# Kernel tuning notes

Measured on AMD Instinct MI355X. Metric: run time of the kernel, lower is better.

Reference implementation:

```python
import jax, jax.numpy as jnp
import numpy as np

N_NODES = 100000
N_EDGES = 3200000
C, H, F = 512, 256, 64


def spmm(edge_row, edge_col, edge_val, Z):
    # (A @ Z)[i] = sum over edges e with row[e]==i of val[e] * Z[col[e]]
    msgs = edge_val[:, None] * Z[edge_col]  # [E, d]
    return jax.ops.segment_sum(msgs, edge_row, num_segments=N_NODES)


def setup_inputs() -> dict:
    key = jax.random.key(0)
    k1, k2, k3, k4, k5, k6, k7 = jax.random.split(key, 7)
    X = jax.random.normal(k1, (N_NODES, C), dtype=jnp.float32)
    edge_row = jax.random.randint(k2, (N_EDGES,), 0, N_NODES, dtype=jnp.int32)
    edge_col = jax.random.randint(k3, (N_EDGES,), 0, N_NODES, dtype=jnp.int32)
    edge_val = jax.random.uniform(k4, (N_EDGES,), dtype=jnp.float32)
    W0 = jax.random.normal(k5, (C, H), dtype=jnp.float32) * (C ** -0.5)
    Wh1 = jax.random.normal(k6, (H, H), dtype=jnp.float32) * (H ** -0.5)
    W1 = jax.random.normal(k7, (H, F), dtype=jnp.float32) * (H ** -0.5)
    return {"X": X, "edge_row": edge_row, "edge_col": edge_col,
            "edge_val": edge_val, "W0": W0, "Wh1": Wh1, "W1": W1}


def reference(X, edge_row, edge_col, edge_val, W0, Wh1, W1):
    # layer 0: relu(A @ (X W0))   (dropout=0 -> identity)
    Z = jax.nn.relu(spmm(edge_row, edge_col, edge_val, X @ W0))
    # hidden layers (num_layers - 2 = 1)
    Z = jax.nn.relu(spmm(edge_row, edge_col, edge_val, Z @ Wh1))
    # output layer: softmax(A @ (Z W1), axis=-1)
    Z = jax.nn.softmax(spmm(edge_row, edge_col, edge_val, Z @ W1), axis=-1)
    return Z
```

## Files before the change

### kernel.cpp

```cpp
#include <hip/hip_runtime.h>
#include <cstdint>
#include <cstddef>


#define SCAN_B 1024

typedef __attribute__((ext_vector_type(8))) short short8_t;
typedef __attribute__((ext_vector_type(4))) short short4_t;
typedef __attribute__((ext_vector_type(4))) float f32x4;

__device__ __forceinline__ short bf16_hi(float x) {
    union { float f; unsigned u; } c; c.f = x;
    return (short)(c.u >> 16);
}
__device__ __forceinline__ float bf16_f32(short h) {
    union { float f; unsigned u; } c; c.u = ((unsigned)(unsigned short)h) << 16;
    return c.f;
}

__device__ __forceinline__ void gload_lds16(const void* g, void* l) {
    __builtin_amdgcn_global_load_lds(
        (const __attribute__((address_space(1))) void*)g,
        (__attribute__((address_space(3))) void*)l, 16, 0, 0);
}

#define GBAR() asm volatile("s_barrier" ::: "memory")
#define LGKM0() asm volatile("s_waitcnt lgkmcnt(0)" ::: "memory")

__device__ __forceinline__ void wait_vm(int n) {
    switch (n) {
        case 0:  asm volatile("s_waitcnt vmcnt(0)"  ::: "memory"); break;
        case 6:  asm volatile("s_waitcnt vmcnt(6)"  ::: "memory"); break;
        case 8:  asm volatile("s_waitcnt vmcnt(8)"  ::: "memory"); break;
        default: asm volatile("s_waitcnt vmcnt(10)" ::: "memory"); break;
    }
}


__global__ __launch_bounds__(256) void count_xcd_k(const int* __restrict__ row,
                                                   int* __restrict__ deg,
                                                   int E, int gsz) {
    const int g = blockIdx.x & 7;
    const int lo = g * gsz, hi = lo + gsz;
    const int tidg = (blockIdx.x >> 3) * 256 + threadIdx.x;
    const int T = (gridDim.x >> 3) * 256;
    const int E4 = E >> 2;
    for (int c = tidg; c < E4; c += T) {
        int4 r = *(const int4*)&row[c * 4];
        if (r.x >= lo && r.x < hi) atomicAdd(&deg[r.x], 1);
        if (r.y >= lo && r.y < hi) atomicAdd(&deg[r.y], 1);
        if (r.z >= lo && r.z < hi) atomicAdd(&deg[r.z], 1);
        if (r.w >= lo && r.w < hi) atomicAdd(&deg[r.w], 1);
    }
    for (int e = E4 * 4 + tidg; e < E; e += T) {
        int r = row[e];
        if (r >= lo && r < hi) atomicAdd(&deg[r], 1);
    }
}

__global__ __launch_bounds__(SCAN_B) void scan1_k(const int* __restrict__ deg,
                                                  int* __restrict__ part,
                                                  int* __restrict__ bsum, int n) {
    __shared__ int buf[SCAN_B];
    int tid = threadIdx.x;
    int i = blockIdx.x * SCAN_B + tid;
    int v = (i < n) ? ((deg[i] + 3) & ~3) : 0;
    buf[tid] = v;
    __syncthreads();
    for (int off = 1; off < SCAN_B; off <<= 1) {
        int y = (tid >= off) ? buf[tid - off] : 0;
        __syncthreads();
        buf[tid] += y;
        __syncthreads();
    }
    if (i < n) part[i] = buf[tid] - v;
    if (tid == SCAN_B - 1) bsum[blockIdx.x] = buf[tid];
}

__global__ __launch_bounds__(128) void scan2_k(int* __restrict__ bsum, int nb) {
    __shared__ int buf[128];
    int tid = threadIdx.x;
    int v = (tid < nb) ? bsum[tid] : 0;
    buf[tid] = v;
    __syncthreads();
    for (int off = 1; off < 128; off <<= 1) {
        int y = (tid >= off) ? buf[tid - off] : 0;
        __syncthreads();
        buf[tid] += y;
        __syncthreads();
    }
    if (tid < nb) bsum[tid] = buf[tid] - v;
    if (tid == nb - 1) bsum[nb] = buf[tid];
}

__global__ __launch_bounds__(SCAN_B) void scan3_k(int* __restrict__ rowptr,
                                                  const int* __restrict__ bsum,
                                                  int* __restrict__ cursor, int n, int nb) {
    int i = blockIdx.x * SCAN_B + threadIdx.x;
    if (i < n) {
        int v = rowptr[i] + bsum[blockIdx.x];
        rowptr[i] = v;
        cursor[i] = v;
    }
    if (i == 0) rowptr[n] = bsum[nb];
}

__global__ __launch_bounds__(256) void scatter_xcd_k(const int* __restrict__ row,
                                                     const int* __restrict__ col,
                                                     const float* __restrict__ val,
                                                     int* __restrict__ cursor,
                                                     int2* __restrict__ ecv,
                                                     int E, int gsz) {
    const int g = blockIdx.x & 7;
    const int lo = g * gsz, hi = lo + gsz;
    const int tidg = (blockIdx.x >> 3) * 256 + threadIdx.x;
    const int T = (gridDim.x >> 3) * 256;
    const int E8 = E >> 3;
    for (int c = tidg; c < E8; c += T) {
        const int e = c * 8;
        int4   r0 = *(const int4*)&row[e];
        int4   r1 = *(const int4*)&row[e + 4];
        int4   c0 = *(const int4*)&col[e];
        int4   c1 = *(const int4*)&col[e + 4];
        float4 v0 = *(const float4*)&val[e];
        float4 v1 = *(const float4*)&val[e + 4];
        int   rr[8] = {r0.x, r0.y, r0.z, r0.w, r1.x, r1.y, r1.z, r1.w};
        int   cc[8] = {c0.x, c0.y, c0.z, c0.w, c1.x, c1.y, c1.z, c1.w};
        float vv[8] = {v0.x, v0.y, v0.z, v0.w, v1.x, v1.y, v1.z, v1.w};
        int p[8];
#pragma unroll
        for (int j = 0; j < 8; ++j)
            p[j] = (rr[j] >= lo && rr[j] < hi) ? atomicAdd(&cursor[rr[j]], 1) : -1;
#pragma unroll
        for (int j = 0; j < 8; ++j)
            if (p[j] >= 0) ecv[p[j]] = make_int2(cc[j], __float_as_int(vv[j]));
    }
    for (int e = E8 * 8 + tidg; e < E; e += T) {
        int r = row[e];
        if (r >= lo && r < hi) {
            int p = atomicAdd(&cursor[r], 1);
            ecv[p] = make_int2(col[e], __float_as_int(val[e]));
        }
    }
}

__global__ __launch_bounds__(256) void pad_fill_k(const int* __restrict__ cursor,
                                                  const int* __restrict__ rowptr,
                                                  int2* __restrict__ ecv, int N) {
    int r = blockIdx.x * 256 + threadIdx.x;
    if (r < N) {
        int q = cursor[r], e = rowptr[r + 1];
        for (; q < e; ++q) ecv[q] = make_int2(0, 0);
    }
}


__global__ void split_w_k(const float* __restrict__ W, short* __restrict__ Bhl,
                          int K, int M) {
    int i = blockIdx.x * 256 + threadIdx.x;
    if (i >= K * M) return;
    int k = i / M, m = i - k * M;
    float x = W[i];
    short hi = bf16_hi(x);
    float r = x - bf16_f32(hi);
    short lo = bf16_hi(r);
    int g = k >> 3, j = k & 7;
    Bhl[(size_t)m * (2 * K) + 16 * g + j] = hi;
    Bhl[(size_t)m * (2 * K) + 16 * g + 8 + j] = lo;
}


template <int K, int BN, int NWR, int NWC, bool AF32>
__global__ __launch_bounds__(256) void gemm_hl(const void* __restrict__ Av,
                                               const short* __restrict__ Bhl,
                                               short* __restrict__ ZQ,
                                               float* __restrict__ scl, int N) {
    constexpr int BM = 64 * NWR;
    constexpr int NF = BN / NWC / 16;
    constexpr int NT = K / 32;
    constexpr int LB = BN / 8 / 4;
    constexpr int LA = AF32 ? 0 : BM / 8 / 4;
    constexpr int L  = LA + LB;
    __shared__ short Ald[2][BM * 64];
    __shared__ short Bld[2][BN * 64];

    const int tid = threadIdx.x, lane = tid & 63, w = tid >> 6;
    const int wr = w / NWC, wc = w % NWC;
    const int row0 = blockIdx.x * BM;
    const int l8 = lane >> 3;
    const int sx = (lane & 7) ^ l8;

    const short* Ahl = (const short*)Av;
    const float* Af  = (const float*)Av;
    const int arow = tid >> 2, aq = tid & 3;
    const int akey = arow & 7;

    f32x4 acc[4][NF] = {};

    auto stageB = [&](int t, int b) {
#pragma unroll
        for (int ch = w; ch < BN / 8; ch += 4)
            gload_lds16(Bhl + (size_t)(ch * 8 + l8) * (2 * K) + (size_t)t * 64 + sx * 8,
                        &Bld[b][ch * 512]);
    };
    auto stageAg = [&](int t, int b) {
#pragma unroll
        for (int ch = w; ch < BM / 8; ch += 4)
            gload_lds16(Ahl + (size_t)(row0 + ch * 8 + l8) * (2 * K) + (size_t)t * 64 + sx * 8,
                        &Ald[b][ch * 512]);
    };
    auto loadAf = [&](int t, float4& x0, float4& x1) {
        int gr = row0 + arow;
        x0 = make_float4(0.f, 0.f, 0.f, 0.f); x1 = x0;
        if (gr < N) {
            x0 = *(const float4*)&Af[(size_t)gr * K + t * 32 + aq * 8];
            x1 = *(const float4*)&Af[(size_t)gr * K + t * 32 + aq * 8 + 4];
        }
    };
    auto writeAf = [&](int b, float4 x0, float4 x1) {
        float f[8] = {x0.x, x0.y, x0.z, x0.w, x1.x, x1.y, x1.z, x1.w};
        short8_t hi, lo;
#pragma unroll
        for (int j = 0; j < 8; ++j) {
            short hh = bf16_hi(f[j]);
            hi[j] = hh;
            lo[j] = bf16_hi(f[j] - bf16_f32(hh));
        }
        *(short8_t*)&Ald[b][arow * 64 + ((2 * aq) ^ akey) * 8] = hi;
        *(short8_t*)&Ald[b][arow * 64 + ((2 * aq + 1) ^ akey) * 8] = lo;
    };

    if constexpr (AF32) {
        float4 a0, a1;
        loadAf(0, a0, a1); writeAf(0, a0, a1); stageB(0, 0);
        loadAf(1, a0, a1); writeAf(1, a0, a1); stageB(1, 1);
        LGKM0();
        wait_vm(8);
    } else {
        stageAg(0, 0); stageB(0, 0);
        stageAg(1, 1); stageB(1, 1);
        wait_vm(L);
    }
    GBAR();

#pragma unroll 2
    for (int t = 0; t < NT; ++t) {
        const int cur = t & 1;

        float4 px0, px1;
        if constexpr (AF32) {
            if (t + 2 < NT) loadAf(t + 2, px0, px1);
        }

        const int sH = (lane >> 4) * 2, sL2 = sH + 1;
        short8_t ah[4], al[4];
#pragma unroll
        for (int m = 0; m < 4; ++m) {
            int rl = wr * 64 + m * 16 + (lane & 15);
            int key = rl & 7;
            ah[m] = *(const short8_t*)&Ald[cur][rl * 64 + (sH ^ key) * 8];
            al[m] = *(const short8_t*)&Ald[cur][rl * 64 + (sL2 ^ key) * 8];
        }
#pragma unroll
        for (int n = 0; n < NF; ++n) {
            int cl = wc * (BN / NWC) + n * 16 + (lane & 15);
            int key = cl & 7;
            short8_t bh = *(const short8_t*)&Bld[cur][cl * 64 + (sH ^ key) * 8];
            short8_t bl = *(const short8_t*)&Bld[cur][cl * 64 + (sL2 ^ key) * 8];
#pragma unroll
            for (int m = 0; m < 4; ++m) {
                acc[m][n] = __builtin_amdgcn_mfma_f32_16x16x32_bf16(ah[m], bh, acc[m][n], 0, 0, 0);
                acc[m][n] = __builtin_amdgcn_mfma_f32_16x16x32_bf16(ah[m], bl, acc[m][n], 0, 0, 0);
                acc[m][n] = __builtin_amdgcn_mfma_f32_16x16x32_bf16(al[m], bh, acc[m][n], 0, 0, 0);
            }
        }

        GBAR();
        if constexpr (AF32) {
            if (t + 2 < NT) {
                writeAf(cur, px0, px1);
                stageB(t + 2, cur);
            }
            LGKM0();
            wait_vm(t + 2 < NT ? 8 : 0);
        } else {
            if (t + 2 < NT) { stageAg(t + 2, cur); stageB(t + 2, cur); }
            wait_vm(t + 2 < NT ? L : 0);
        }
        GBAR();
    }

    const int lg = lane >> 4, lc = lane & 15;
    float* maxb = (float*)&Ald[0][0];
    float rmax[4][4];
#pragma unroll
    for (int m = 0; m < 4; ++m)
#pragma unroll
        for (int r = 0; r < 4; ++r) {
            float v = 0.f;
#pragma unroll
            for (int n = 0; n < NF; ++n) v = fmaxf(v, fabsf(acc[m][n][r]));
#pragma unroll
            for (int o = 8; o >= 1; o >>= 1) v = fmaxf(v, __shfl_xor(v, o));
            rmax[m][r] = v;
        }
    if constexpr (NWC > 1) {
        __syncthreads();
        if (lc == 0)
#pragma unroll
            for (int m = 0; m < 4; ++m)
#pragma unroll
                for (int r = 0; r < 4; ++r)
                    maxb[(wr * 64 + m * 16 + lg * 4 + r) * NWC + wc] = rmax[m][r];
        __syncthreads();
    }
#pragma unroll
    for (int m = 0; m < 4; ++m)
#pragma unroll
        for (int r = 0; r < 4; ++r) {
            int rl = wr * 64 + m * 16 + lg * 4 + r;
            float v = rmax[m][r];
            if constexpr (NWC > 1) {
                v = maxb[rl * NWC];
#pragma unroll
                for (int q = 1; q < NWC; ++q) v = fmaxf(v, maxb[rl * NWC + q]);
            }
            int grow = row0 + rl;
            if (grow < N) {
                float inv = (v > 0.f) ? 32767.f / v : 0.f;
                if (lc == 0 && wc == 0) scl[grow] = v * (1.f / 32767.f);
#pragma unroll
                for (int n = 0; n < NF; ++n)
                    ZQ[(size_t)grow * BN + wc * (BN / NWC) + n * 16 + lc] =
                        (short)rintf(acc[m][n][r] * inv);
            }
        }
}


__global__ __launch_bounds__(256) void spmm_agg256_k(const int* __restrict__ rowptr,
                                                     const int2* __restrict__ ecv,
                                                     const short* __restrict__ Q,
                                                     const float* __restrict__ scl,
                                                     short* __restrict__ Zhl, int N) {
    int row = blockIdx.x * 4 + (threadIdx.x >> 6);
    if (row >= N) return;
    const int lane = threadIdx.x & 63;
    const int half = lane >> 5;
    const int l32 = lane & 31;
    int s = rowptr[row], e = rowptr[row + 1];
    const short8_t* Qv = (const short8_t*)Q;
    f32x4 a0 = {0.f, 0.f, 0.f, 0.f}, a1 = a0;
    for (int i = s; i < e; i += 4) {
        int4 A = *(const int4*)(ecv + i);
        int4 B = *(const int4*)(ecv + i + 2);
        int   cA = half ? A.z : A.x;
        float wA = __int_as_float(half ? A.w : A.y) * scl[cA];
        int   cB = half ? B.z : B.x;
        float wB = __int_as_float(half ? B.w : B.y) * scl[cB];
        short8_t qA = Qv[(size_t)cA * 32 + l32];
        short8_t qB = Qv[(size_t)cB * 32 + l32];
#pragma unroll
        for (int j = 0; j < 4; ++j) {
            a0[j] = fmaf(wA, (float)qA[j], a0[j]);
            a1[j] = fmaf(wA, (float)qA[j + 4], a1[j]);
            a0[j] = fmaf(wB, (float)qB[j], a0[j]);
            a1[j] = fmaf(wB, (float)qB[j + 4], a1[j]);
        }
    }
#pragma unroll
    for (int j = 0; j < 4; ++j) {
        a0[j] += __shfl_xor(a0[j], 32);
        a1[j] += __shfl_xor(a1[j], 32);
    }
    if (half == 0) {
        short8_t hi, lo;
#pragma unroll
        for (int j = 0; j < 4; ++j) {
            float r0 = fmaxf(a0[j], 0.f), r1 = fmaxf(a1[j], 0.f);
            short h0 = bf16_hi(r0), h1 = bf16_hi(r1);
            hi[j] = h0; hi[j + 4] = h1;
            lo[j] = bf16_hi(r0 - bf16_f32(h0));
            lo[j + 4] = bf16_hi(r1 - bf16_f32(h1));
        }
        size_t base = (size_t)row * 512 + l32 * 16;
        *(short8_t*)&Zhl[base] = hi;
        *(short8_t*)&Zhl[base + 8] = lo;
    }
}

__global__ __launch_bounds__(256) void spmm_softmax64_k(const int* __restrict__ rowptr,
                                                        const int2* __restrict__ ecv,
                                                        const short* __restrict__ Q,
                                                        const float* __restrict__ scl,
                                                        float* __restrict__ out, int N) {
    int row = blockIdx.x * 4 + (threadIdx.x >> 6);
    if (row >= N) return;
    const int lane = threadIdx.x & 63;
    const int q = lane >> 4;
    const int l16 = lane & 15;
    int s = rowptr[row], e = rowptr[row + 1];
    const short4_t* Qv = (const short4_t*)Q;
    f32x4 acc = {0.f, 0.f, 0.f, 0.f};
    for (int i = s; i < e; i += 4) {
        int4 A = *(const int4*)(ecv + i);
        int4 B = *(const int4*)(ecv + i + 2);
        int c = (q & 2) ? ((q & 1) ? B.z : B.x) : ((q & 1) ? A.z : A.x);
        int wbits = (q & 2) ? ((q & 1) ? B.w : B.y) : ((q & 1) ? A.w : A.y);
        float wv = __int_as_float(wbits) * scl[c];
        short4_t z = Qv[(size_t)c * 16 + l16];
#pragma unroll
        for (int j = 0; j < 4; ++j) acc[j] = fmaf(wv, (float)z[j], acc[j]);
    }
#pragma unroll
    for (int j = 0; j < 4; ++j) {
        acc[j] += __shfl_xor(acc[j], 16);
        acc[j] += __shfl_xor(acc[j], 32);
    }
    float m = fmaxf(fmaxf(acc[0], acc[1]), fmaxf(acc[2], acc[3]));
#pragma unroll
    for (int o = 8; o >= 1; o >>= 1) m = fmaxf(m, __shfl_xor(m, o));
    float p0 = __expf(acc[0] - m), p1 = __expf(acc[1] - m);
    float p2 = __expf(acc[2] - m), p3 = __expf(acc[3] - m);
    float ssum = p0 + p1 + p2 + p3;
#pragma unroll
    for (int o = 8; o >= 1; o >>= 1) ssum += __shfl_xor(ssum, o);
    if (q == 0) {
        float inv = 1.f / ssum;
        float4 o4 = make_float4(p0 * inv, p1 * inv, p2 * inv, p3 * inv);
        *(float4*)&out[(size_t)row * 64 + l16 * 4] = o4;
    }
}


extern "C" void kernel_launch(void* const* d_in, const int* in_sizes, int n_in,
                              void* d_out, int out_size, void* d_ws, size_t ws_size,
                              hipStream_t stream) {
    const float* X        = (const float*)d_in[0];
    const int*   edge_row = (const int*)d_in[1];
    const int*   edge_col = (const int*)d_in[2];
    const float* edge_val = (const float*)d_in[3];
    const float* W0       = (const float*)d_in[4];
    const float* Wh1      = (const float*)d_in[5];
    const float* W1       = (const float*)d_in[6];

    const int C = 512, H = 256, F = 64;
    const int N = in_sizes[0] / C;
    const int E = in_sizes[1];
    const int EPAD = E + 4 * N + 64;

    size_t off = 0;
    auto alloc = [&](size_t bytes) -> void* {
        void* p = (char*)d_ws + off;
        off += (bytes + 255) & ~(size_t)255;
        return p;
    };
    short* Zhl    = (short*)alloc((size_t)N * 2 * H * sizeof(short));
    short* ZQ     = (short*)alloc((size_t)N * H * sizeof(short));
    float* scl    = (float*)alloc((size_t)N * sizeof(float));
    int*   deg    = (int*)alloc((size_t)N * sizeof(int));
    int*   rowptr = (int*)alloc((size_t)(N + 1) * sizeof(int));
    int*   cursor = (int*)alloc((size_t)N * sizeof(int));
    int*   bsum   = (int*)alloc(129 * sizeof(int));
    int2*  ecv    = (int2*)alloc((size_t)EPAD * sizeof(int2));
    short* Bhl0   = (short*)alloc((size_t)H * 2 * C * sizeof(short));
    short* Bhl1   = (short*)alloc((size_t)H * 2 * H * sizeof(short));
    short* Bhl2   = (short*)alloc((size_t)F * 2 * H * sizeof(short));
    (void)ws_size;

    hipMemsetAsync(deg, 0, (size_t)N * sizeof(int), stream);
    const int gsz = (N + 7) / 8;
    count_xcd_k<<<2048, 256, 0, stream>>>(edge_row, deg, E, gsz);
    int nb = (N + SCAN_B - 1) / SCAN_B;
    scan1_k<<<nb, SCAN_B, 0, stream>>>(deg, rowptr, bsum, N);
    scan2_k<<<1, 128, 0, stream>>>(bsum, nb);
    scan3_k<<<nb, SCAN_B, 0, stream>>>(rowptr, bsum, cursor, N, nb);
    scatter_xcd_k<<<2048, 256, 0, stream>>>(edge_row, edge_col, edge_val,
                                            cursor, ecv, E, gsz);
    pad_fill_k<<<(N + 255) / 256, 256, 0, stream>>>(cursor, rowptr, ecv, N);

    split_w_k<<<(C * H + 255) / 256, 256, 0, stream>>>(W0, Bhl0, C, H);
    split_w_k<<<(H * H + 255) / 256, 256, 0, stream>>>(Wh1, Bhl1, H, H);
    split_w_k<<<(H * F + 255) / 256, 256, 0, stream>>>(W1, Bhl2, H, F);

    const int g64  = (N + 63) / 64;
    const int g128 = (N + 127) / 128;
    const int rg   = (N + 3) / 4;

    gemm_hl<512, 256, 1, 4, true><<<g64, 256, 0, stream>>>(X, Bhl0, ZQ, scl, N);
    spmm_agg256_k<<<rg, 256, 0, stream>>>(rowptr, ecv, ZQ, scl, Zhl, N);
    gemm_hl<256, 256, 1, 4, false><<<g64, 256, 0, stream>>>(Zhl, Bhl1, ZQ, scl, N);
    spmm_agg256_k<<<rg, 256, 0, stream>>>(rowptr, ecv, ZQ, scl, Zhl, N);
    gemm_hl<256, 64, 2, 2, false><<<g128, 256, 0, stream>>>(Zhl, Bhl2, ZQ, scl, N);
    spmm_softmax64_k<<<rg, 256, 0, stream>>>(rowptr, ecv, ZQ, scl,
                                             (float*)d_out, N);
}
```

Measured before the change: 1.115 ms.

## Switch hidden and output GEMMs to split int8 MFMA with per-row scales

Replaces the bf16 hi/lo split representation for the second and third GEMMs with a 16-bit fixed-point value split into two int8 halves, for both the aggregated activations and the weights. Each side carries a per-row or per-column scale. Products use i8 MFMA 16x16x64 with three partial products, and the results are rescaled into the existing int16 quantized output. This halves the activation bytes written by the SpMM and read by the GEMM, and uses faster int8 matrix instructions, at the cost of per-row quantization error and extra epilogue arithmetic.

```diff
diff --git a/kernel.cpp b/kernel.cpp
--- a/kernel.cpp
+++ b/kernel.cpp
@@ -8,6 +8,7 @@
 typedef __attribute__((ext_vector_type(8))) short short8_t;
 typedef __attribute__((ext_vector_type(4))) short short4_t;
 typedef __attribute__((ext_vector_type(4))) float f32x4;
+typedef __attribute__((ext_vector_type(4))) int i32x4;
 
 __device__ __forceinline__ short bf16_hi(float x) {
     union { float f; unsigned u; } c; c.f = x;
@@ -170,6 +171,29 @@
 }
 
 
+__global__ __launch_bounds__(64) void split_w_i8(const float* __restrict__ W,
+                                                 signed char* __restrict__ B8,
+                                                 float* __restrict__ sB,
+                                                 int K, int M) {
+    int m = blockIdx.x;
+    int lane = threadIdx.x;
+    float mx = 0.f;
+    for (int k = lane; k < K; k += 64) mx = fmaxf(mx, fabsf(W[(size_t)k * M + m]));
+#pragma unroll
+    for (int o = 32; o >= 1; o >>= 1) mx = fmaxf(mx, __shfl_xor(mx, o));
+    float qs = (mx > 0.f) ? 32512.f / mx : 0.f;
+    for (int k = lane; k < K; k += 64) {
+        int q = (int)rintf(W[(size_t)k * M + m] * qs);
+        int h = (q + 128) >> 8;
+        int l = q - (h << 8);
+        size_t base = (size_t)m * (2 * K) + (size_t)(k >> 6) * 128;
+        B8[base + (k & 63)] = (signed char)h;
+        B8[base + 64 + (k & 63)] = (signed char)l;
+    }
+    if (lane == 0) sB[m] = mx * (1.f / 32512.f);
+}
+
+
 template <int K, int BN, int NWR, int NWC, bool AF32>
 __global__ __launch_bounds__(256) void gemm_hl(const void* __restrict__ Av,
                                                const short* __restrict__ Bhl,
@@ -338,11 +362,145 @@
 }
 
 
+template <int K, int BN, int NWR, int NWC>
+__global__ __launch_bounds__(256) void gemm_i8(const signed char* __restrict__ A8,
+                                               const float* __restrict__ sA,
+                                               const signed char* __restrict__ B8,
+                                               const float* __restrict__ sB,
+                                               short* __restrict__ ZQ,
+                                               float* __restrict__ scl, int N) {
+    constexpr int BM = 64 * NWR;
+    constexpr int NF = BN / NWC / 16;
+    constexpr int NT = K / 64;
+    constexpr int LA = BM / 8 / 4;
+    constexpr int LB = BN / 8 / 4;
+    constexpr int L  = LA + LB;
+    __shared__ int Ald[2][BM * 32];
+    __shared__ int Bld[2][BN * 32];
+
+    const int tid = threadIdx.x, lane = tid & 63, w = tid >> 6;
+    const int wr = w / NWC, wc = w % NWC;
+    const int row0 = blockIdx.x * BM;
+    const int l8 = lane >> 3;
+    const int sx = (lane & 7) ^ l8;
+
+    i32x4 acc1[4][NF] = {};
+    i32x4 acc2[4][NF] = {};
+
+    auto stageA = [&](int t, int b) {
+#pragma unroll
+        for (int ch = w; ch < BM / 8; ch += 4)
+            gload_lds16(A8 + (size_t)(row0 + ch * 8 + l8) * (2 * K) + t * 128 + sx * 16,
+                        (char*)&Ald[b][0] + ch * 1024);
+    };
+    auto stageB = [&](int t, int b) {
+#pragma unroll
+        for (int ch = w; ch < BN / 8; ch += 4)
+            gload_lds16(B8 + (size_t)(ch * 8 + l8) * (2 * K) + t * 128 + sx * 16,
+                        (char*)&Bld[b][0] + ch * 1024);
+    };
+
+    stageA(0, 0); stageB(0, 0);
+    stageA(1, 1); stageB(1, 1);
+    wait_vm(L);
+    GBAR();
+
+#pragma unroll 2
+    for (int t = 0; t < NT; ++t) {
+        const int cur = t & 1;
+        const int g = lane >> 4;
+        i32x4 ah[4], al[4];
+#pragma unroll
+        for (int m = 0; m < 4; ++m) {
+            int rl = wr * 64 + m * 16 + (lane & 15);
+            int key = rl & 7;
+            ah[m] = *(const i32x4*)((const char*)&Ald[cur][0] + rl * 128 + ((g ^ key) * 16));
+            al[m] = *(const i32x4*)((const char*)&Ald[cur][0] + rl * 128 + (((g + 4) ^ key) * 16));
+        }
+#pragma unroll
+        for (int n = 0; n < NF; ++n) {
+            int cl = wc * (BN / NWC) + n * 16 + (lane & 15);
+            int key = cl & 7;
+            i32x4 bh = *(const i32x4*)((const char*)&Bld[cur][0] + cl * 128 + ((g ^ key) * 16));
+            i32x4 bl = *(const i32x4*)((const char*)&Bld[cur][0] + cl * 128 + (((g + 4) ^ key) * 16));
+#pragma unroll
+            for (int m = 0; m < 4; ++m) {
+                acc1[m][n] = __builtin_amdgcn_mfma_i32_16x16x64_i8(ah[m], bh, acc1[m][n], 0, 0, 0);
+                acc2[m][n] = __builtin_amdgcn_mfma_i32_16x16x64_i8(ah[m], bl, acc2[m][n], 0, 0, 0);
+                acc2[m][n] = __builtin_amdgcn_mfma_i32_16x16x64_i8(al[m], bh, acc2[m][n], 0, 0, 0);
+            }
+        }
+        GBAR();
+        if (t + 2 < NT) { stageA(t + 2, cur); stageB(t + 2, cur); }
+        wait_vm(t + 2 < NT ? L : 0);
+        GBAR();
+    }
+
+    const int lg = lane >> 4, lc = lane & 15;
+    float sbv[NF];
+#pragma unroll
+    for (int n = 0; n < NF; ++n) sbv[n] = sB[wc * (BN / NWC) + n * 16 + lc];
+
+    float* maxb = (float*)&Ald[0][0];
+    float rmax[4][4];
+#pragma unroll
+    for (int m = 0; m < 4; ++m)
+#pragma unroll
+        for (int r = 0; r < 4; ++r) {
+            float v = 0.f;
+#pragma unroll
+            for (int n = 0; n < NF; ++n) {
+                float cf = sbv[n] * (65536.f * (float)acc1[m][n][r] +
+                                     256.f * (float)acc2[m][n][r]);
+                v = fmaxf(v, fabsf(cf));
+            }
+#pragma unroll
+            for (int o = 8; o >= 1; o >>= 1) v = fmaxf(v, __shfl_xor(v, o));
+            rmax[m][r] = v;
+        }
+    if constexpr (NWC > 1) {
+        __syncthreads();
+        if (lc == 0)
+#pragma unroll
+            for (int m = 0; m < 4; ++m)
+#pragma unroll
+                for (int r = 0; r < 4; ++r)
+                    maxb[(wr * 64 + m * 16 + lg * 4 + r) * NWC + wc] = rmax[m][r];
+        __syncthreads();
+    }
+#pragma unroll
+    for (int m = 0; m < 4; ++m)
+#pragma unroll
+        for (int r = 0; r < 4; ++r) {
+            int rl = wr * 64 + m * 16 + lg * 4 + r;
+            float v = rmax[m][r];
+            if constexpr (NWC > 1) {
+                v = maxb[rl * NWC];
+#pragma unroll
+                for (int q = 1; q < NWC; ++q) v = fmaxf(v, maxb[rl * NWC + q]);
+            }
+            int grow = row0 + rl;
+            if (grow < N) {
+                float inv = (v > 0.f) ? 32767.f / v : 0.f;
+                if (lc == 0 && wc == 0) scl[grow] = sA[grow] * v * (1.f / 32767.f);
+#pragma unroll
+                for (int n = 0; n < NF; ++n) {
+                    float cf = sbv[n] * (65536.f * (float)acc1[m][n][r] +
+                                         256.f * (float)acc2[m][n][r]);
+                    ZQ[(size_t)grow * BN + wc * (BN / NWC) + n * 16 + lc] =
+                        (short)rintf(cf * inv);
+                }
+            }
+        }
+}
+
+
 __global__ __launch_bounds__(256) void spmm_agg256_k(const int* __restrict__ rowptr,
                                                      const int2* __restrict__ ecv,
                                                      const short* __restrict__ Q,
                                                      const float* __restrict__ scl,
-                                                     short* __restrict__ Zhl, int N) {
+                                                     signed char* __restrict__ ZA8,
+                                                     float* __restrict__ sza, int N) {
     int row = blockIdx.x * 4 + (threadIdx.x >> 6);
     if (row >= N) return;
     const int lane = threadIdx.x & 63;
@@ -373,19 +531,32 @@
         a0[j] += __shfl_xor(a0[j], 32);
         a1[j] += __shfl_xor(a1[j], 32);
     }
+    float r0[4], r1[4];
+    float mx = 0.f;
+#pragma unroll
+    for (int j = 0; j < 4; ++j) {
+        r0[j] = fmaxf(a0[j], 0.f);
+        r1[j] = fmaxf(a1[j], 0.f);
+        mx = fmaxf(mx, fmaxf(r0[j], r1[j]));
+    }
+#pragma unroll
+    for (int o = 16; o >= 1; o >>= 1) mx = fmaxf(mx, __shfl_xor(mx, o));
+    float qs = (mx > 0.f) ? 32512.f / mx : 0.f;
     if (half == 0) {
-        short8_t hi, lo;
-#pragma unroll
-        for (int j = 0; j < 4; ++j) {
-            float r0 = fmaxf(a0[j], 0.f), r1 = fmaxf(a1[j], 0.f);
-            short h0 = bf16_hi(r0), h1 = bf16_hi(r1);
-            hi[j] = h0; hi[j + 4] = h1;
-            lo[j] = bf16_hi(r0 - bf16_f32(h0));
-            lo[j + 4] = bf16_hi(r1 - bf16_f32(h1));
-        }
-        size_t base = (size_t)row * 512 + l32 * 16;
-        *(short8_t*)&Zhl[base] = hi;
-        *(short8_t*)&Zhl[base + 8] = lo;
+        unsigned long long hw = 0, lw = 0;
+#pragma unroll
+        for (int j = 0; j < 8; ++j) {
+            float rv = (j < 4) ? r0[j] : r1[j - 4];
+            int q = (int)rintf(rv * qs);
+            int h = (q + 128) >> 8;
+            int l = q - (h << 8);
+            hw |= (unsigned long long)(unsigned char)(signed char)h << (8 * j);
+            lw |= (unsigned long long)(unsigned char)(signed char)l << (8 * j);
+        }
+        size_t base = (size_t)row * 512 + (size_t)(l32 >> 3) * 128 + (l32 & 7) * 8;
+        *(unsigned long long*)(ZA8 + base) = hw;
+        *(unsigned long long*)(ZA8 + base + 64) = lw;
+        if (lane == 0) sza[row] = mx * (1.f / 32512.f);
     }
 }
 
@@ -455,17 +626,20 @@
         off += (bytes + 255) & ~(size_t)255;
         return p;
     };
-    short* Zhl    = (short*)alloc((size_t)N * 2 * H * sizeof(short));
+    signed char* ZA8 = (signed char*)alloc((size_t)N * 2 * H);
     short* ZQ     = (short*)alloc((size_t)N * H * sizeof(short));
     float* scl    = (float*)alloc((size_t)N * sizeof(float));
+    float* sza    = (float*)alloc((size_t)N * sizeof(float));
     int*   deg    = (int*)alloc((size_t)N * sizeof(int));
     int*   rowptr = (int*)alloc((size_t)(N + 1) * sizeof(int));
     int*   cursor = (int*)alloc((size_t)N * sizeof(int));
     int*   bsum   = (int*)alloc(129 * sizeof(int));
     int2*  ecv    = (int2*)alloc((size_t)EPAD * sizeof(int2));
     short* Bhl0   = (short*)alloc((size_t)H * 2 * C * sizeof(short));
-    short* Bhl1   = (short*)alloc((size_t)H * 2 * H * sizeof(short));
-    short* Bhl2   = (short*)alloc((size_t)F * 2 * H * sizeof(short));
+    signed char* B1i8 = (signed char*)alloc((size_t)H * 2 * H);
+    signed char* B2i8 = (signed char*)alloc((size_t)F * 2 * H);
+    float* sb1    = (float*)alloc((size_t)H * sizeof(float));
+    float* sb2    = (float*)alloc((size_t)F * sizeof(float));
     (void)ws_size;
 
     hipMemsetAsync(deg, 0, (size_t)N * sizeof(int), stream);
@@ -480,18 +654,18 @@
     pad_fill_k<<<(N + 255) / 256, 256, 0, stream>>>(cursor, rowptr, ecv, N);
 
     split_w_k<<<(C * H + 255) / 256, 256, 0, stream>>>(W0, Bhl0, C, H);
-    split_w_k<<<(H * H + 255) / 256, 256, 0, stream>>>(Wh1, Bhl1, H, H);
-    split_w_k<<<(H * F + 255) / 256, 256, 0, stream>>>(W1, Bhl2, H, F);
+    split_w_i8<<<H, 64, 0, stream>>>(Wh1, B1i8, sb1, H, H);
+    split_w_i8<<<F, 64, 0, stream>>>(W1, B2i8, sb2, H, F);
 
     const int g64  = (N + 63) / 64;
     const int g128 = (N + 127) / 128;
     const int rg   = (N + 3) / 4;
 
     gemm_hl<512, 256, 1, 4, true><<<g64, 256, 0, stream>>>(X, Bhl0, ZQ, scl, N);
-    spmm_agg256_k<<<rg, 256, 0, stream>>>(rowptr, ecv, ZQ, scl, Zhl, N);
-    gemm_hl<256, 256, 1, 4, false><<<g64, 256, 0, stream>>>(Zhl, Bhl1, ZQ, scl, N);
-    spmm_agg256_k<<<rg, 256, 0, stream>>>(rowptr, ecv, ZQ, scl, Zhl, N);
-    gemm_hl<256, 64, 2, 2, false><<<g128, 256, 0, stream>>>(Zhl, Bhl2, ZQ, scl, N);
+    spmm_agg256_k<<<rg, 256, 0, stream>>>(rowptr, ecv, ZQ, scl, ZA8, sza, N);
+    gemm_i8<256, 256, 1, 4><<<g64, 256, 0, stream>>>(ZA8, sza, B1i8, sb1, ZQ, scl, N);
+    spmm_agg256_k<<<rg, 256, 0, stream>>>(rowptr, ecv, ZQ, scl, ZA8, sza, N);
+    gemm_i8<256, 64, 2, 2><<<g128, 256, 0, stream>>>(ZA8, sza, B2i8, sb2, ZQ, scl, N);
     spmm_softmax64_k<<<rg, 256, 0, stream>>>(rowptr, ecv, ZQ, scl,
                                              (float*)d_out, N);
 }
```

After: 1.103 ms. Within noise of the previous version (-1.0%).
